# Kernel tuning notes

Hardware: AMD Instinct MI355X
Metric: run time of the kernel (lower is better)

Reference implementation:

```python
import jax, jax.numpy as jnp
import numpy as np

IN_FEATURES = 3
MAPPING_SIZE = 128
FF_SCALE = 10.0
HIDDEN = 512
HIDDEN_LAYERS = 5
OUT_FEATURES = 3
OMEGA0 = 30.0
TWO_PI = 2.0 * np.pi


def setup_inputs() -> dict:
    key = jax.random.key(0)
    ks = jax.random.split(key, 10)
    B, L = 1, 262144
    coords = jax.random.uniform(ks[0], (B, L, IN_FEATURES), jnp.float32, -1.0, 1.0)
    # Fourier feature projection (random Gaussian buffer, scale=10)
    B_ff = jax.random.normal(ks[1], (IN_FEATURES, MAPPING_SIZE), jnp.float32) * FF_SCALE
    ff_dim = 2 * MAPPING_SIZE  # 256
    # First sine layer: is_first=True -> U(-1/in, 1/in)
    W_first = jax.random.uniform(ks[2], (HIDDEN, ff_dim), jnp.float32, -1.0 / ff_dim, 1.0 / ff_dim)
    b_first = jax.random.uniform(ks[3], (HIDDEN,), jnp.float32, -1.0 / np.sqrt(ff_dim), 1.0 / np.sqrt(ff_dim))
    # Hidden sine layers: U(-sqrt(6/in)/omega0, +)
    wh = np.sqrt(6.0 / HIDDEN) / OMEGA0
    W_hidden = jax.random.uniform(ks[4], (HIDDEN_LAYERS, HIDDEN, HIDDEN), jnp.float32, -wh, wh)
    b_hidden = jax.random.uniform(ks[5], (HIDDEN_LAYERS, HIDDEN), jnp.float32, -1.0 / np.sqrt(HIDDEN), 1.0 / np.sqrt(HIDDEN))
    # Final linear: U(-sqrt(6/hidden)/omega0, +)
    W_out = jax.random.uniform(ks[6], (OUT_FEATURES, HIDDEN), jnp.float32, -wh, wh)
    b_out = jax.random.uniform(ks[7], (OUT_FEATURES,), jnp.float32, -1.0 / np.sqrt(HIDDEN), 1.0 / np.sqrt(HIDDEN))
    return {"coords": coords, "B_ff": B_ff, "W_first": W_first, "b_first": b_first,
            "W_hidden": W_hidden, "b_hidden": b_hidden, "W_out": W_out, "b_out": b_out}


def reference(coords, B_ff, W_first, b_first, W_hidden, b_hidden, W_out, b_out):
    # Fourier feature encoding: [B,L,3] -> [B,L,256]
    proj = TWO_PI * (coords @ B_ff)
    h = jnp.concatenate([jnp.sin(proj), jnp.cos(proj)], axis=-1)
    # First sine layer
    h = jnp.sin(OMEGA0 * (jnp.einsum('bli,oi->blo', h, W_first) + b_first))
    # Hidden sine layers (stacked weights, scanned)
    def step(h, wb):
        w, b = wb
        return jnp.sin(OMEGA0 * (jnp.einsum('bli,oi->blo', h, w) + b)), None
    h, _ = jax.lax.scan(step, h, (W_hidden, b_hidden))
    # Outermost linear
    return jnp.einsum('bli,oi->blo', h, W_out) + b_out
```

## Files before the change

### kernel.cpp

```cpp
#include <hip/hip_runtime.h>


#define L_TOTAL 262144
#define TOK 128
#define THREADS 512
#define C_SC 4.77464829275686f

typedef _Float16 f16x8 __attribute__((ext_vector_type(8)));
typedef _Float16 f16x4 __attribute__((ext_vector_type(4)));
typedef float    f32x4 __attribute__((ext_vector_type(4)));

#define N1 (512 * 256)
#define N2 (N1 + 5 * 512 * 512)
#define N3 (N2 + 16 * 512)
#define NBIAS 3072

__global__ void convert_weights(const float* __restrict__ Wf,
                                const float* __restrict__ Wh,
                                const float* __restrict__ Wo,
                                const float* __restrict__ bf,
                                const float* __restrict__ bh,
                                _Float16* __restrict__ o,
                                float* __restrict__ biasC) {
  int i = blockIdx.x * blockDim.x + threadIdx.x;
  if (i < N3) {
    float v;
    if (i < N1) {
      const int blk = i >> 9, w = i & 511;
      const int lane = w >> 3, e = w & 7;
      const int mt = blk >> 3, ks = blk & 7;
      const int row = mt * 16 + (lane & 15);
      const int col = ks * 32 + (lane >> 4) * 8 + e;
      v = Wf[row * 256 + col];
    } else if (i < N2) {
      int j = i - N1;
      const int l = j >> 18;
      j &= (1 << 18) - 1;
      const int blk = j >> 9, w = j & 511;
      const int lane = w >> 3, e = w & 7;
      const int mt = blk >> 4, ks = blk & 15;
      const int row = mt * 16 + (lane & 15);
      const int col = ks * 32 + (lane >> 4) * 8 + e;
      v = Wh[l * (512 * 512) + row * 512 + col];
    } else {
      const int r = (i - N2) >> 9, c = (i - N2) & 511;
      v = (r < 3) ? Wo[r * 512 + c] : 0.0f;
    }
    o[i] = (_Float16)v;
  } else if (i < N3 + NBIAS) {
    int j = i - N3;
    biasC[j] = (j < 512 ? bf[j] : bh[j - 512]) * C_SC;
  }
}

__device__ __forceinline__ int h_elem(int chunk, int token) {
  return (chunk * 128 + token) * 8;
}

template <int K>
__device__ __forceinline__ void sine_layer(const _Float16* __restrict__ W,
                                           const float* __restrict__ biasC,
                                           _Float16* hb, int lane, int lr,
                                           int lg, int m0) {
  constexpr int KS = K / 32;
  f32x4 acc[4][8];
#pragma unroll
  for (int mt = 0; mt < 4; ++mt)
#pragma unroll
    for (int nt = 0; nt < 8; ++nt)
      acc[mt][nt] = (f32x4){0.f, 0.f, 0.f, 0.f};

  const _Float16* wb[4];
#pragma unroll
  for (int mt = 0; mt < 4; ++mt)
    wb[mt] = &W[(((m0 >> 4) + mt) * KS) * 512 + lane * 8];

  f16x8 a[3][4], b[2][8];
#pragma unroll
  for (int mt = 0; mt < 4; ++mt) a[0][mt] = *(const f16x8*)(wb[mt]);
#pragma unroll
  for (int mt = 0; mt < 4; ++mt) a[1][mt] = *(const f16x8*)(wb[mt] + 512);
#pragma unroll
  for (int nt = 0; nt < 8; ++nt)
    b[0][nt] = *(const f16x8*)&hb[h_elem(lg, nt * 16 + lr)];

#pragma unroll
  for (int ks = 0; ks < KS; ++ks) {
    const int cur = ks & 1;
    const int ai = ks % 3;
    if (ks + 1 < KS) {
#pragma unroll
      for (int nt = 0; nt < 8; ++nt)
        b[cur ^ 1][nt] =
            *(const f16x8*)&hb[h_elem((ks + 1) * 4 + lg, nt * 16 + lr)];
    }
    if (ks + 2 < KS) {
#pragma unroll
      for (int mt = 0; mt < 4; ++mt)
        a[(ks + 2) % 3][mt] = *(const f16x8*)(wb[mt] + (ks + 2) * 512);
    }
#pragma unroll
    for (int mt = 0; mt < 4; ++mt)
#pragma unroll
      for (int nt = 0; nt < 8; ++nt)
        acc[mt][nt] = __builtin_amdgcn_mfma_f32_16x16x32_f16(
            a[ai][mt], b[cur][nt], acc[mt][nt], 0, 0, 0);
  }
  __syncthreads();

#pragma unroll
  for (int mt = 0; mt < 4; ++mt) {
    const int ob = m0 + mt * 16 + lg * 4;
    const f32x4 bb = *(const f32x4*)&biasC[ob];
    const int wbase = (ob >> 3) * 128 * 8 + (ob & 7);
#pragma unroll
    for (int nt = 0; nt < 8; ++nt) {
      f16x4 hv;
#pragma unroll
      for (int r = 0; r < 4; ++r) {
        float pre = fmaf(acc[mt][nt][r], C_SC, bb[r]);
        hv[r] = (_Float16)__builtin_amdgcn_sinf(__builtin_amdgcn_fractf(pre));
      }
      *(f16x4*)&hb[wbase + (nt * 16 + lr) * 8] = hv;
    }
  }
  __syncthreads();
}

__global__ __launch_bounds__(THREADS, 2) void siren_kernel(
    const float* __restrict__ coords, const float* __restrict__ bff,
    const float* __restrict__ biasC, const float* __restrict__ b_out,
    const _Float16* __restrict__ wf, const _Float16* __restrict__ wh,
    const _Float16* __restrict__ wo, float* __restrict__ out) {
  extern __shared__ _Float16 hb[];
  const int tid = threadIdx.x;
  const int t0 = blockIdx.x * TOK;

  {
    const int t = tid & 127;
    const int q = tid >> 7;
    const float c0 = coords[(t0 + t) * 3 + 0];
    const float c1 = coords[(t0 + t) * 3 + 1];
    const float c2 = coords[(t0 + t) * 3 + 2];
#pragma unroll
    for (int cb = 0; cb < 4; ++cb) {
      f16x8 sv, cv;
#pragma unroll
      for (int e = 0; e < 8; ++e) {
        const int j = q * 32 + cb * 8 + e;
        float r = fmaf(c0, bff[j], fmaf(c1, bff[128 + j], c2 * bff[256 + j]));
        float fr = __builtin_amdgcn_fractf(r);
        sv[e] = (_Float16)__builtin_amdgcn_sinf(fr);
        cv[e] = (_Float16)__builtin_amdgcn_cosf(fr);
      }
      *(f16x8*)&hb[h_elem(q * 4 + cb, t)] = sv;
      *(f16x8*)&hb[h_elem(16 + q * 4 + cb, t)] = cv;
    }
  }
  __syncthreads();

  const int lane = tid & 63;
  const int lr = lane & 15;
  const int lg = lane >> 4;
  const int m0 = (tid >> 6) * 64;

  sine_layer<256>(wf, biasC, hb, lane, lr, lg, m0);
#pragma unroll 1
  for (int l = 0; l < 5; ++l)
    sine_layer<512>(wh + l * (512 * 512), biasC + 512 + l * 512, hb, lane, lr,
                    lg, m0);

  {
    const int wave = tid >> 6;
    f32x4 acc = {0.f, 0.f, 0.f, 0.f};
#pragma unroll
    for (int ks = 0; ks < 16; ++ks) {
      f16x8 a = *(const f16x8*)&wo[lr * 512 + ks * 32 + lg * 8];
      f16x8 b = *(const f16x8*)&hb[h_elem(ks * 4 + lg, wave * 16 + lr)];
      acc = __builtin_amdgcn_mfma_f32_16x16x32_f16(a, b, acc, 0, 0, 0);
    }
    if (lg == 0) {
      const int t = t0 + wave * 16 + lr;
      out[t * 3 + 0] = acc[0] + b_out[0];
      out[t * 3 + 1] = acc[1] + b_out[1];
      out[t * 3 + 2] = acc[2] + b_out[2];
    }
  }
}

extern "C" void kernel_launch(void* const* d_in, const int* in_sizes, int n_in,
                              void* d_out, int out_size, void* d_ws,
                              size_t ws_size, hipStream_t stream) {
  const float* coords = (const float*)d_in[0];
  const float* bff    = (const float*)d_in[1];
  const float* Wf     = (const float*)d_in[2];
  const float* bf     = (const float*)d_in[3];
  const float* Wh     = (const float*)d_in[4];
  const float* bh     = (const float*)d_in[5];
  const float* Wo     = (const float*)d_in[6];
  const float* bo     = (const float*)d_in[7];
  float* out = (float*)d_out;

  _Float16* w16 = (_Float16*)d_ws;
  float* biasC = (float*)(w16 + N3);

  convert_weights<<<(N3 + NBIAS + 255) / 256, 256, 0, stream>>>(
      Wf, Wh, Wo, bf, bh, w16, biasC);

  const size_t lds_bytes = 64 * 128 * 8 * sizeof(_Float16);
  siren_kernel<<<L_TOTAL / TOK, THREADS, lds_bytes, stream>>>(
      coords, bff, biasC, bo, w16, w16 + N1, w16 + N2, out);
}
```

Baseline: 740.3 us.

## Prefetch next layer's weights across barrier and use lighter LDS-only barriers

Loads the first two k-slices of the next layer's weight fragments before the epilogue barrier, so the global-load latency for the next layer overlaps the sine epilogue and the barrier. The weight register ring grows from 3 to 4 slots, and the bias loads are hoisted before the MMA loop. __syncthreads is replaced with an inline s_waitcnt lgkmcnt(0) plus s_barrier, which skips waiting on outstanding global (vmcnt) loads. The cost is more VGPR pressure, which could cause spills under launch_bounds(512,2), and the barrier now relies on only LDS traffic needing to be ordered.

```diff
diff --git a/kernel.cpp b/kernel.cpp
--- a/kernel.cpp
+++ b/kernel.cpp
@@ -14,6 +14,9 @@
 #define N2 (N1 + 5 * 512 * 512)
 #define N3 (N2 + 16 * 512)
 #define NBIAS 3072
+
+#define BARRIER() \
+  __asm__ __volatile__("s_waitcnt lgkmcnt(0)\n\ts_barrier" ::: "memory")
 
 __global__ void convert_weights(const float* __restrict__ Wf,
                                 const float* __restrict__ Wh,
@@ -57,11 +60,13 @@
   return (chunk * 128 + token) * 8;
 }
 
-template <int K>
+template <int K, int KN>
 __device__ __forceinline__ void sine_layer(const _Float16* __restrict__ W,
+                                           const _Float16* __restrict__ Wnext,
                                            const float* __restrict__ biasC,
-                                           _Float16* hb, int lane, int lr,
-                                           int lg, int m0) {
+                                           _Float16* hb, f16x8 (&a)[4][4],
+                                           int lane, int lr, int lg,
+                                           int mtb) {
   constexpr int KS = K / 32;
   f32x4 acc[4][8];
 #pragma unroll
@@ -70,16 +75,18 @@
     for (int nt = 0; nt < 8; ++nt)
       acc[mt][nt] = (f32x4){0.f, 0.f, 0.f, 0.f};
 
+  const int m0 = mtb * 16;
+  f32x4 bb[4];
+#pragma unroll
+  for (int mt = 0; mt < 4; ++mt)
+    bb[mt] = *(const f32x4*)&biasC[m0 + mt * 16 + lg * 4];
+
   const _Float16* wb[4];
 #pragma unroll
   for (int mt = 0; mt < 4; ++mt)
-    wb[mt] = &W[(((m0 >> 4) + mt) * KS) * 512 + lane * 8];
-
-  f16x8 a[3][4], b[2][8];
-#pragma unroll
-  for (int mt = 0; mt < 4; ++mt) a[0][mt] = *(const f16x8*)(wb[mt]);
-#pragma unroll
-  for (int mt = 0; mt < 4; ++mt) a[1][mt] = *(const f16x8*)(wb[mt] + 512);
+    wb[mt] = &W[((mtb + mt) * KS) * 512 + lane * 8];
+
+  f16x8 b[2][8];
 #pragma unroll
   for (int nt = 0; nt < 8; ++nt)
     b[0][nt] = *(const f16x8*)&hb[h_elem(lg, nt * 16 + lr)];
@@ -87,7 +94,6 @@
 #pragma unroll
   for (int ks = 0; ks < KS; ++ks) {
     const int cur = ks & 1;
-    const int ai = ks % 3;
     if (ks + 1 < KS) {
 #pragma unroll
       for (int nt = 0; nt < 8; ++nt)
@@ -97,34 +103,44 @@
     if (ks + 2 < KS) {
 #pragma unroll
       for (int mt = 0; mt < 4; ++mt)
-        a[(ks + 2) % 3][mt] = *(const f16x8*)(wb[mt] + (ks + 2) * 512);
+        a[(ks + 2) & 3][mt] = *(const f16x8*)(wb[mt] + (ks + 2) * 512);
     }
 #pragma unroll
     for (int mt = 0; mt < 4; ++mt)
 #pragma unroll
       for (int nt = 0; nt < 8; ++nt)
         acc[mt][nt] = __builtin_amdgcn_mfma_f32_16x16x32_f16(
-            a[ai][mt], b[cur][nt], acc[mt][nt], 0, 0, 0);
-  }
-  __syncthreads();
+            a[ks & 3][mt], b[cur][nt], acc[mt][nt], 0, 0, 0);
+  }
+
+  {
+    constexpr int KSN = KN / 32;
+#pragma unroll
+    for (int mt = 0; mt < 4; ++mt) {
+      const _Float16* wbn = &Wnext[((mtb + mt) * KSN) * 512 + lane * 8];
+      a[0][mt] = *(const f16x8*)(wbn);
+      a[1][mt] = *(const f16x8*)(wbn + 512);
+    }
+  }
+
+  BARRIER();
 
 #pragma unroll
   for (int mt = 0; mt < 4; ++mt) {
     const int ob = m0 + mt * 16 + lg * 4;
-    const f32x4 bb = *(const f32x4*)&biasC[ob];
-    const int wbase = (ob >> 3) * 128 * 8 + (ob & 7);
+    const int wbase = (ob >> 3) * 1024 + (ob & 7);
 #pragma unroll
     for (int nt = 0; nt < 8; ++nt) {
       f16x4 hv;
 #pragma unroll
       for (int r = 0; r < 4; ++r) {
-        float pre = fmaf(acc[mt][nt][r], C_SC, bb[r]);
+        float pre = fmaf(acc[mt][nt][r], C_SC, bb[mt][r]);
         hv[r] = (_Float16)__builtin_amdgcn_sinf(__builtin_amdgcn_fractf(pre));
       }
       *(f16x4*)&hb[wbase + (nt * 16 + lr) * 8] = hv;
     }
   }
-  __syncthreads();
+  BARRIER();
 }
 
 __global__ __launch_bounds__(THREADS, 2) void siren_kernel(
@@ -135,6 +151,19 @@
   extern __shared__ _Float16 hb[];
   const int tid = threadIdx.x;
   const int t0 = blockIdx.x * TOK;
+
+  const int lane = tid & 63;
+  const int lr = lane & 15;
+  const int lg = lane >> 4;
+  const int mtb = (tid >> 6) * 4;
+
+  f16x8 a[4][4];
+#pragma unroll
+  for (int mt = 0; mt < 4; ++mt) {
+    const _Float16* wbn = &wf[((mtb + mt) * 8) * 512 + lane * 8];
+    a[0][mt] = *(const f16x8*)(wbn);
+    a[1][mt] = *(const f16x8*)(wbn + 512);
+  }
 
   {
     const int t = tid & 127;
@@ -157,27 +186,25 @@
       *(f16x8*)&hb[h_elem(16 + q * 4 + cb, t)] = cv;
     }
   }
-  __syncthreads();
-
-  const int lane = tid & 63;
-  const int lr = lane & 15;
-  const int lg = lane >> 4;
-  const int m0 = (tid >> 6) * 64;
-
-  sine_layer<256>(wf, biasC, hb, lane, lr, lg, m0);
+  BARRIER();
+
+  sine_layer<256, 512>(wf, wh, biasC, hb, a, lane, lr, lg, mtb);
 #pragma unroll 1
-  for (int l = 0; l < 5; ++l)
-    sine_layer<512>(wh + l * (512 * 512), biasC + 512 + l * 512, hb, lane, lr,
-                    lg, m0);
+  for (int l = 0; l < 5; ++l) {
+    const _Float16* W = wh + l * (512 * 512);
+    const _Float16* Wn = (l < 4) ? (W + 512 * 512) : W;
+    sine_layer<512, 512>(W, Wn, biasC + 512 + l * 512, hb, a, lane, lr, lg,
+                         mtb);
+  }
 
   {
     const int wave = tid >> 6;
     f32x4 acc = {0.f, 0.f, 0.f, 0.f};
 #pragma unroll
     for (int ks = 0; ks < 16; ++ks) {
-      f16x8 a = *(const f16x8*)&wo[lr * 512 + ks * 32 + lg * 8];
-      f16x8 b = *(const f16x8*)&hb[h_elem(ks * 4 + lg, wave * 16 + lr)];
-      acc = __builtin_amdgcn_mfma_f32_16x16x32_f16(a, b, acc, 0, 0, 0);
+      f16x8 av = *(const f16x8*)&wo[lr * 512 + ks * 32 + lg * 8];
+      f16x8 bv = *(const f16x8*)&hb[h_elem(ks * 4 + lg, wave * 16 + lr)];
+      acc = __builtin_amdgcn_mfma_f32_16x16x32_f16(av, bv, acc, 0, 0, 0);
     }
     if (lg == 0) {
       const int t = t0 + wave * 16 + lr;
```

Result: slower. 894.6 us (+20.8%).
